# Kernel tuning notes

Measured on AMD Instinct MI355X. Metric: run time of the kernel, lower is better.

The kernel has to match this reference:

```python
import jax, jax.numpy as jnp
import numpy as np

B, N, DIM = 2, 512, 512
HEADS, DIM_HEAD, MAX_LEN = 8, 64, 1024


def _skew(QEr):
    # pad last dim on the left by 1, reshape (n, n+1) -> (n+1, n), drop first row
    padded = jnp.pad(QEr, ((0, 0), (0, 0), (0, 0), (1, 0)))
    b, h, r, c = padded.shape
    return padded.reshape(b, h, c, r)[:, :, 1:, :]


def _fft_multiply_parallel(A, x):
    # A: [b,h,n,n] decay matrix; x: [b,h,n,d]
    b, h, n, d = x.shape
    # y = [last column of A, first row of A] -> [b,h,2n]
    y = jnp.concatenate([A[:, :, :, -1], A[:, :, 0, :]], axis=-1)
    v = jnp.concatenate([x, jnp.zeros_like(x)], axis=-2)  # zero-pad rows n -> 2n
    # Faithful to the original torch code: fftn over ALL axes (incl. batch/head),
    # then ifft over the LAST axis only, then slice back to n rows.
    H = jnp.fft.fftn(y)[:, :, :, None] * jnp.fft.fftn(v)
    return jnp.fft.ifft(H)[:, :, :n, :]


def _forward(x, Wq, Wk, Wv, Er):
    b, n, _ = x.shape

    def split_heads(t):
        return t.reshape(b, n, HEADS, DIM_HEAD).transpose(0, 2, 1, 3)  # [b,h,n,d]

    q = split_heads(x @ Wq)
    k = split_heads(x @ Wk)
    v = split_heads(x @ Wv)
    # global (Frobenius) norm over the full tensor, as torch.norm(t)
    q = q / jnp.linalg.norm(q)
    k = k / jnp.linalg.norm(k)
    q_ = jax.nn.elu(q)
    k_ = jax.nn.elu(k)

    Er_t = Er[MAX_LEN - n:, :].T        # [d, n]
    QEr = q @ Er_t                       # [b,h,n,n]
    c = jnp.exp(_skew(QEr))              # relative-position decay, [b,h,n,n]

    a_1 = jnp.einsum('bhnx,bhny->bhnxy', k_, v).reshape(b, HEADS, n, DIM_HEAD * DIM_HEAD)
    d_2 = _fft_multiply_parallel(c, k_)                                   # [b,h,n,d] complex
    d_1 = _fft_multiply_parallel(c, a_1).reshape(b, HEADS, n, DIM_HEAD, DIM_HEAD)

    top = jnp.einsum('bhnx,bhnyz->bhnz', q_, d_1)    # complex [b,h,n,d]
    bottom = jnp.einsum('bhnx,bhny->bhny', q_, d_2)  # complex [b,h,n,d]
    return top / bottom


def setup_inputs() -> dict:
    key = jax.random.key(0)
    k1, k2, k3, k4, k5 = jax.random.split(key, 5)
    s = jnp.float32(1.0 / np.sqrt(DIM))
    return {
        'x': jax.random.normal(k1, (B, N, DIM), dtype=jnp.float32),
        'Wq': jax.random.normal(k2, (DIM, HEADS * DIM_HEAD), dtype=jnp.float32) * s,
        'Wk': jax.random.normal(k3, (DIM, HEADS * DIM_HEAD), dtype=jnp.float32) * s,
        'Wv': jax.random.normal(k4, (DIM, HEADS * DIM_HEAD), dtype=jnp.float32) * s,
        'Er': jax.random.normal(k5, (MAX_LEN, DIM_HEAD), dtype=jnp.float32),
    }


def reference(x, Wq, Wk, Wv, Er):
    return _forward(x, Wq, Wk, Wv, Er)
```

## Files before the change

kernel.cpp:

```cpp
#include <hip/hip_runtime.h>
#include <math.h>


#define DIMX 512
#define NPOS 512
#define PADIDX(m) ((m) + ((m) >> 4))

typedef unsigned short ushort_t;
typedef unsigned int uint_t;
typedef __bf16 bf16x8 __attribute__((ext_vector_type(8)));
typedef float floatx4 __attribute__((ext_vector_type(4)));

static __device__ inline ushort_t f2bf(float f) {
    uint_t u = __float_as_uint(f);
    u = u + 0x7FFFu + ((u >> 16) & 1u);
    return (ushort_t)(u >> 16);
}
static __device__ inline float bf2f(ushort_t h) {
    return __uint_as_float(((uint_t)h) << 16);
}

__global__ __launch_bounds__(256)
void convx_kernel(const float* __restrict__ x,
                  ushort_t* __restrict__ xh, ushort_t* __restrict__ xl)
{
    const int idx4 = blockIdx.x * 256 + threadIdx.x;
    const float4 v = ((const float4*)x)[idx4];
    ushort_t h[4], l[4];
    const float vf[4] = {v.x, v.y, v.z, v.w};
    #pragma unroll
    for (int e = 0; e < 4; ++e) {
        h[e] = f2bf(vf[e]);
        l[e] = f2bf(vf[e] - bf2f(h[e]));
    }
    ushort_t* ph = xh + (size_t)idx4 * 4;
    ushort_t* pl = xl + (size_t)idx4 * 4;
    #pragma unroll
    for (int e = 0; e < 4; ++e) { ph[e] = h[e]; pl[e] = l[e]; }
}

__global__ __launch_bounds__(256)
void convw_kernel(const float* __restrict__ Wk, const float* __restrict__ Wv,
                  ushort_t* __restrict__ wth, ushort_t* __restrict__ wtl)
{
    const int blk = blockIdx.x;
    const int s  = blk >> 8;
    const int kt = (blk >> 4) & 15;
    const int nt = blk & 15;
    const int t  = threadIdx.x;
    const int c  = t & 31, r4 = t >> 5;
    const float* __restrict__ W = s ? Wv : Wk;
    __shared__ float tile[32][33];

    #pragma unroll
    for (int i = 0; i < 4; ++i) {
        const int row = r4 + i * 8;
        tile[row][c] = W[(size_t)(kt * 32 + row) * 512 + nt * 32 + c];
    }
    __syncthreads();
    #pragma unroll
    for (int i = 0; i < 4; ++i) {
        const int nl = r4 + i * 8;
        const float v = tile[c][nl];
        const ushort_t h = f2bf(v);
        const ushort_t l = f2bf(v - bf2f(h));
        const size_t o = (size_t)(s * 512 + nt * 32 + nl) * 512 + kt * 32 + c;
        wth[o] = h;
        wtl[o] = l;
    }
}

__global__ __launch_bounds__(256)
void gemm_mfma_kernel(const ushort_t* __restrict__ xh, const ushort_t* __restrict__ xl,
                      const ushort_t* __restrict__ wth, const ushort_t* __restrict__ wtl,
                      float* __restrict__ K, float* __restrict__ V,
                      float* __restrict__ partials)
{
    const int blk = blockIdx.x;
    const int ct = blk >> 5;
    const int rt = blk & 31;
    const int t = threadIdx.x;
    const int w = t >> 6, lane = t & 63;
    const int qd = lane >> 4, lm = lane & 15;
    const int mrow  = rt * 32 + (w >> 1) * 16 + lm;
    const int ncol0 = ct * 64 + (w & 1) * 32;
    const size_t aoff  = (size_t)mrow * 512 + qd * 8;
    const size_t boff0 = (size_t)(ncol0 + lm) * 512 + qd * 8;
    const size_t boff1 = (size_t)(ncol0 + 16 + lm) * 512 + qd * 8;

    floatx4 acc0 = {0.f, 0.f, 0.f, 0.f};
    floatx4 acc1 = {0.f, 0.f, 0.f, 0.f};

    #pragma unroll
    for (int ks = 0; ks < 16; ++ks) {
        const int k0 = ks * 32;
        const bf16x8 Ah  = *(const bf16x8*)&xh [aoff  + k0];
        const bf16x8 Al  = *(const bf16x8*)&xl [aoff  + k0];
        const bf16x8 B0h = *(const bf16x8*)&wth[boff0 + k0];
        const bf16x8 B0l = *(const bf16x8*)&wtl[boff0 + k0];
        const bf16x8 B1h = *(const bf16x8*)&wth[boff1 + k0];
        const bf16x8 B1l = *(const bf16x8*)&wtl[boff1 + k0];
        acc0 = __builtin_amdgcn_mfma_f32_16x16x32_bf16(Ah, B0h, acc0, 0, 0, 0);
        acc0 = __builtin_amdgcn_mfma_f32_16x16x32_bf16(Ah, B0l, acc0, 0, 0, 0);
        acc0 = __builtin_amdgcn_mfma_f32_16x16x32_bf16(Al, B0h, acc0, 0, 0, 0);
        acc1 = __builtin_amdgcn_mfma_f32_16x16x32_bf16(Ah, B1h, acc1, 0, 0, 0);
        acc1 = __builtin_amdgcn_mfma_f32_16x16x32_bf16(Ah, B1l, acc1, 0, 0, 0);
        acc1 = __builtin_amdgcn_mfma_f32_16x16x32_bf16(Al, B1h, acc1, 0, 0, 0);
    }

    __shared__ float red[4];
    float ss = 0.f;
    const int orow0 = rt * 32 + (w >> 1) * 16 + qd * 4;
    float* __restrict__ O = (ct < 8) ? K : V;
    const int cb = (ct < 8) ? 0 : 512;
    const int c0 = ncol0 + lm - cb;
    #pragma unroll
    for (int r = 0; r < 4; ++r) {
        const size_t row = orow0 + r;
        const float v0 = acc0[r], v1 = acc1[r];
        O[row * 512 + c0]      = v0;
        O[row * 512 + c0 + 16] = v1;
        if (ct < 8) ss += v0 * v0 + v1 * v1;
    }
    #pragma unroll
    for (int off = 32; off > 0; off >>= 1)
        ss += __shfl_down(ss, off, 64);
    if (lane == 0) red[w] = ss;
    __syncthreads();
    if (t == 0) partials[blk] = red[0] + red[1] + red[2] + red[3];
}

__global__ __launch_bounds__(256)
void gemm_kv_kernel(const float* __restrict__ x,
                    const float* __restrict__ Wk,
                    const float* __restrict__ Wv,
                    float* __restrict__ K,
                    float* __restrict__ V,
                    float* __restrict__ partials)
{
    const int blk  = blockIdx.x;
    const int sel  = (blk >> 2) & 1;
    const int cg   = blk & 3;
    const int rt   = blk >> 3;
    const int row0 = rt * 16;
    const int col0 = cg * 128;
    const int t    = threadIdx.x;
    const int tc   = t & 31;
    const int tr   = t >> 5;
    const float* __restrict__ W   = sel ? Wv : Wk;
    float* __restrict__       Out = sel ? V  : K;

    __shared__ float xs[16][DIMX];
    __shared__ float red[4];

    #pragma unroll
    for (int j = 0; j < 8; ++j) {
        const int f = t + j * 256;
        const int row = f >> 7, c4 = f & 127;
        *(float4*)&xs[row][c4 * 4] = *(const float4*)&x[(size_t)(row0 + row) * DIMX + c4 * 4];
    }
    __syncthreads();

    const float* Wb = W + col0 + tc * 4;
    float4 wA[8], wB[8];
    #pragma unroll
    for (int j = 0; j < 8; ++j) wA[j] = *(const float4*)&Wb[(size_t)(j) * DIMX];
    #pragma unroll
    for (int j = 0; j < 8; ++j) wB[j] = *(const float4*)&Wb[(size_t)(8 + j) * DIMX];

    float acc[2][4] = {{0,0,0,0},{0,0,0,0}};
    const int r0 = tr * 2;

    #define COMPUTE_CHUNK(WREG, CH)                                            \
        {   float4 xv0a = *(const float4*)&xs[r0][(CH) * 8];                   \
            float4 xv0b = *(const float4*)&xs[r0][(CH) * 8 + 4];               \
            float4 xv1a = *(const float4*)&xs[r0 + 1][(CH) * 8];               \
            float4 xv1b = *(const float4*)&xs[r0 + 1][(CH) * 8 + 4];           \
            _Pragma("unroll")                                                  \
            for (int kk = 0; kk < 4; ++kk) {                                   \
                const float x0 = (&xv0a.x)[kk], x1 = (&xv1a.x)[kk];            \
                _Pragma("unroll")                                              \
                for (int cc = 0; cc < 4; ++cc) {                               \
                    acc[0][cc] = fmaf(x0, (&WREG[kk].x)[cc], acc[0][cc]);      \
                    acc[1][cc] = fmaf(x1, (&WREG[kk].x)[cc], acc[1][cc]);      \
                } }                                                            \
            _Pragma("unroll")                                                  \
            for (int kk = 0; kk < 4; ++kk) {                                   \
                const float x0 = (&xv0b.x)[kk], x1 = (&xv1b.x)[kk];            \
                _Pragma("unroll")                                              \
                for (int cc = 0; cc < 4; ++cc) {                               \
                    acc[0][cc] = fmaf(x0, (&WREG[kk + 4].x)[cc], acc[0][cc]);  \
                    acc[1][cc] = fmaf(x1, (&WREG[kk + 4].x)[cc], acc[1][cc]);  \
                } } }

    for (int ch = 0; ch < 64; ch += 2) {
        COMPUTE_CHUNK(wA, ch)
        if (ch < 62) {
            #pragma unroll
            for (int j = 0; j < 8; ++j)
                wA[j] = *(const float4*)&Wb[(size_t)((ch + 2) * 8 + j) * DIMX];
        }
        COMPUTE_CHUNK(wB, ch + 1)
        if (ch < 62) {
            #pragma unroll
            for (int j = 0; j < 8; ++j)
                wB[j] = *(const float4*)&Wb[(size_t)((ch + 3) * 8 + j) * DIMX];
        }
    }
    #undef COMPUTE_CHUNK

    float ss = 0.f;
    #pragma unroll
    for (int i = 0; i < 2; ++i) {
        const int row = row0 + r0 + i;
        const float4 o = make_float4(acc[i][0], acc[i][1], acc[i][2], acc[i][3]);
        *(float4*)&Out[(size_t)row * DIMX + col0 + tc * 4] = o;
        ss += o.x * o.x + o.y * o.y + o.z * o.z + o.w * o.w;
    }
    if (sel == 0) {
        #pragma unroll
        for (int off = 32; off > 0; off >>= 1)
            ss += __shfl_down(ss, off, 64);
        if ((t & 63) == 0) red[t >> 6] = ss;
        __syncthreads();
        if (t == 0) partials[blk] = red[0] + red[1] + red[2] + red[3];
    } else {
        if (t == 0) partials[blk] = 0.f;
    }
}

__device__ __constant__ float C8[8] = {
    1.f, 0.70710678118654752440f, 0.f, -0.70710678118654752440f,
   -1.f, -0.70710678118654752440f, 0.f, 0.70710678118654752440f };
__device__ __constant__ float S8[8] = {
    0.f, -0.70710678118654752440f, -1.f, -0.70710678118654752440f,
    0.f,  0.70710678118654752440f,  1.f,  0.70710678118654752440f };

__global__ __launch_bounds__(256)
void stage1_kernel(const float* __restrict__ K,
                   const float* __restrict__ V,
                   const float* __restrict__ partials,
                   float2* __restrict__ Gk,
                   float2* __restrict__ Gp)
{
    const int m = blockIdx.x;
    const int t = threadIdx.x;
    __shared__ float kk[2][8][64];
    __shared__ float pp[2][8][64];
    __shared__ float skp[16][4];
    __shared__ float sk[2][8];
    __shared__ float sred[4];

    float p = partials[t] + partials[t + 256];
    #pragma unroll
    for (int off = 32; off > 0; off >>= 1)
        p += __shfl_down(p, off, 64);
    if ((t & 63) == 0) sred[t >> 6] = p;
    __syncthreads();
    const float scale = (float)(1.0 / sqrt((double)sred[0] + (double)sred[1] +
                                           (double)sred[2] + (double)sred[3]));

    for (int e = t; e < 1024; e += 256) {
        const int b = e >> 9, rem = e & 511, h = rem >> 6, z = rem & 63;
        const size_t src = (size_t)(b * 512 + m) * DIMX + h * 64 + z;
        const float kv = K[src] * scale;
        kk[b][h][z] = kv > 0.f ? kv : expm1f(kv);
        pp[b][h][z] = V[src];
    }
    __syncthreads();
    if (t < 64) {
        const int bh = t >> 2, q = t & 3;
        float s = 0.f;
        #pragma unroll
        for (int zz = 0; zz < 16; ++zz) s += kk[bh >> 3][bh & 7][q * 16 + zz];
        skp[bh][q] = s;
    }
    __syncthreads();
    if (t < 16) sk[t >> 3][t & 7] = skp[t][0] + skp[t][1] + skp[t][2] + skp[t][3];
    __syncthreads();
    for (int e = t; e < 1024; e += 256) {
        const int b = e >> 9, rem = e & 511, h = rem >> 6, z = rem & 63;
        pp[b][h][z] *= sk[b][h];
    }
    __syncthreads();

    for (int e2 = t; e2 < 512; e2 += 256) {
        const int be = e2 >> 5;
        const int zp = e2 & 31;
        const int beta = be >> 3, eta = be & 7;
        float4 rk, rp;
        #pragma unroll
        for (int zz = 0; zz < 2; ++zz) {
            const int z = zp * 2 + zz;
            float gkr = 0.f, gki = 0.f, gpr = 0.f, gpi = 0.f;
            #pragma unroll
            for (int b = 0; b < 2; ++b) {
                const float sgn = (beta & b) ? -1.f : 1.f;
                #pragma unroll
                for (int h = 0; h < 8; ++h) {
                    const int ph = (eta * h) & 7;
                    const float cr = C8[ph], ci = S8[ph];
                    const float a = kk[b][h][z] * sgn;
                    gkr = fmaf(a, cr, gkr); gki = fmaf(a, ci, gki);
                    const float p2 = pp[b][h][z] * sgn;
                    gpr = fmaf(p2, cr, gpr); gpi = fmaf(p2, ci, gpi);
                }
            }
            if (zz == 0) { rk.x = gkr; rk.y = gki; rp.x = gpr; rp.y = gpi; }
            else         { rk.z = gkr; rk.w = gki; rp.z = gpr; rp.w = gpi; }
        }
        const size_t o = ((size_t)be * NPOS + m) * 64 + zp * 2;
        *(float4*)&Gk[o] = rk;
        *(float4*)&Gp[o] = rp;
    }
}

__global__ __launch_bounds__(256)
void fft_div_kernel(const float2* __restrict__ Gk,
                    const float2* __restrict__ Gp,
                    float* __restrict__ out, int out_cplx)
{
    const int blk = blockIdx.x;
    const int j  = blk & 7;
    const int l  = (blk >> 3) & 3;
    const int be = blk >> 5;
    const int zg = j * 4 + l;
    const int t  = threadIdx.x;

    __shared__ float2 g[4][1088];
    __shared__ float2 w[544];

    for (int jj = t; jj < 512; jj += 256) {
        double s, cc;
        sincos(-6.2831853071795864769 * (double)jj / 1024.0, &s, &cc);
        w[PADIDX(jj)] = make_float2((float)cc, (float)s);
    }
    __syncthreads();

    for (int e = t; e < 1024; e += 256) {
        const int a = e >> 9;
        const int m = e & 511;
        const float4 v4 = *(const float4*)&(a ? Gp : Gk)[((size_t)be * NPOS + m) * 64 + zg * 2];
        const float2 v0 = make_float2(v4.x, v4.y);
        const float2 v1 = make_float2(v4.z, v4.w);
        const float2 tw = w[PADIDX(m)];
        g[a * 2 + 0][PADIDX(m)] = v0;
        g[a * 2 + 1][PADIDX(m)] = v1;
        g[a * 2 + 0][PADIDX(m + 512)] = make_float2(v0.x * tw.x - v0.y * tw.y,
                                                    v0.x * tw.y + v0.y * tw.x);
        g[a * 2 + 1][PADIDX(m + 512)] = make_float2(v1.x * tw.x - v1.y * tw.y,
                                                    v1.x * tw.y + v1.y * tw.x);
    }
    __syncthreads();

    #pragma unroll
    for (int s = 1; s <= 9; ++s) {
        const int S = 512 >> s;
        const int lg = 9 - s;
        #pragma unroll
        for (int q = 0; q < 8; ++q) {
            const int B    = t + 256 * q;
            const int arr  = B >> 9;
            const int beta = B & 511;
            const int jb   = beta & (S - 1);
            const int seg  = beta >> lg;
            const int u    = (seg << (lg + 1)) + jb;
            const int v    = u + S;
            const float2 tw = w[PADIDX(jb << s)];
            const float2 A  = g[arr][PADIDX(u)];
            const float2 Bb = g[arr][PADIDX(v)];
            g[arr][PADIDX(u)] = make_float2(A.x + Bb.x, A.y + Bb.y);
            const float sr = A.x - Bb.x, si = A.y - Bb.y;
            g[arr][PADIDX(v)] = make_float2(sr * tw.x - si * tw.y,
                                            sr * tw.y + si * tw.x);
        }
        __syncthreads();
    }

    for (int e2 = t; e2 < 512; e2 += 256) {
        const int i  = e2;
        const int pi = PADIDX(2 * i);
        const int mu = (int)(__brev((unsigned)i) >> 23);
        float4 res;
        #pragma unroll
        for (int zi = 0; zi < 2; ++zi) {
            const float2 D  = g[zi][pi];
            const float2 Nm = g[2 + zi][pi];
            const float inv = 1.f / (D.x * D.x + D.y * D.y);
            const float rr = (Nm.x * D.x + Nm.y * D.y) * inv;
            const float ri = (Nm.y * D.x - Nm.x * D.y) * inv;
            if (zi == 0) { res.x = rr; res.y = ri; }
            else         { res.z = rr; res.w = ri; }
        }
        const size_t o = ((size_t)be * NPOS + mu) * 64 + zg * 2;
        if (out_cplx) {
            *(float4*)&((float2*)out)[o] = res;
        } else {
            out[o]     = res.x;
            out[o + 1] = res.z;
        }
    }
}

__global__ __launch_bounds__(256)
void mdft_fallback_kernel(const float2* __restrict__ Gk,
                          const float2* __restrict__ Gp,
                          float* __restrict__ out,
                          int out_cplx)
{
    const int blk = blockIdx.x;
    const int be = blk >> 6, z = blk & 63;
    const int t = threadIdx.x;
    __shared__ float2 gk[512];
    __shared__ float2 gp[512];
    __shared__ float2 w[1024];

    for (int m = t; m < 512; m += 256) {
        const size_t idx = ((size_t)be * NPOS + m) * 64 + z;
        gk[m] = Gk[idx];
        gp[m] = Gp[idx];
    }
    for (int jj = t; jj < 1024; jj += 256) {
        double s, c;
        sincos(-6.2831853071795864769 * (double)jj / 1024.0, &s, &c);
        w[jj] = make_float2((float)c, (float)s);
    }
    __syncthreads();

    #pragma unroll
    for (int half = 0; half < 2; ++half) {
        const int mu = t + half * 256;
        double dr = 0.0, di = 0.0, nr = 0.0, ni = 0.0;
        int idx = 0;
        for (int m = 0; m < 512; ++m) {
            const float2 tw = w[idx];
            idx = (idx + mu) & 1023;
            const float2 a = gk[m];
            dr += (double)(a.x * tw.x - a.y * tw.y);
            di += (double)(a.x * tw.y + a.y * tw.x);
            const float2 p = gp[m];
            nr += (double)(p.x * tw.x - p.y * tw.y);
            ni += (double)(p.x * tw.y + p.y * tw.x);
        }
        const double dmag = dr * dr + di * di;
        const double orr = (nr * dr + ni * di) / dmag;
        const double oii = (ni * dr - nr * di) / dmag;
        const size_t o = ((size_t)be * NPOS + mu) * 64 + z;
        if (out_cplx) {
            out[2 * o]     = (float)orr;
            out[2 * o + 1] = (float)oii;
        } else {
            out[o] = (float)orr;
        }
    }
}

extern "C" void kernel_launch(void* const* d_in, const int* in_sizes, int n_in,
                              void* d_out, int out_size, void* d_ws, size_t ws_size,
                              hipStream_t stream)
{
    const float* x  = (const float*)d_in[0];
    const float* Wk = (const float*)d_in[2];
    const float* Wv = (const float*)d_in[3];
    float* out = (float*)d_out;

    char* ws = (char*)d_ws;
    float*  K    = (float*)(ws);
    float*  V    = (float*)(ws + (size_t)2097152);
    float2* Gk   = (float2*)(ws + (size_t)4194304);
    float*  part = (float*)(ws + (size_t)8388608);
    const int out_cplx = (out_size >= 2 * 2 * 8 * 512 * 64) ? 1 : 0;

    const bool ws_big = (ws_size >= (size_t)20971520);
    float2* Gp = ws_big ? (float2*)(ws + (size_t)8390656)
                        : (float2*)d_out;

    if (ws_big) {
        ushort_t* xh  = (ushort_t*)(ws + (size_t)16777216);
        ushort_t* xl  = (ushort_t*)(ws + (size_t)17825792);
        ushort_t* wth = (ushort_t*)(ws + (size_t)18874368);
        ushort_t* wtl = (ushort_t*)(ws + (size_t)19922944);
        hipLaunchKernelGGL(convx_kernel, dim3(512), dim3(256), 0, stream,
                           x, xh, xl);
        hipLaunchKernelGGL(convw_kernel, dim3(512), dim3(256), 0, stream,
                           Wk, Wv, wth, wtl);
        hipLaunchKernelGGL(gemm_mfma_kernel, dim3(512), dim3(256), 0, stream,
                           xh, xl, wth, wtl, K, V, part);
        hipLaunchKernelGGL(stage1_kernel, dim3(512), dim3(256), 0, stream,
                           K, V, part, Gk, Gp);
        hipLaunchKernelGGL(fft_div_kernel, dim3(512), dim3(256), 0, stream,
                           Gk, Gp, out, out_cplx);
    } else {
        hipLaunchKernelGGL(gemm_kv_kernel, dim3(512), dim3(256), 0, stream,
                           x, Wk, Wv, K, V, part);
        hipLaunchKernelGGL(stage1_kernel, dim3(512), dim3(256), 0, stream,
                           K, V, part, Gk, Gp);
        hipLaunchKernelGGL(mdft_fallback_kernel, dim3(1024), dim3(256), 0, stream,
                           Gk, Gp, out, out_cplx);
    }
}
```

Before: 113.0 us.

## Fuse five-stage pipeline into one cooperative kernel with grid syncs

Merges the conversion, MFMA GEMM, stage1 and FFT-divide kernels into a single cooperative kernel that separates phases with grid-wide syncs and shares one statically sized shared-memory buffer. The aim is to remove four kernel launch gaps and their inter-kernel drain and refill. The trade-off is that every phase now runs under the largest shared-memory footprint and register budget, and grid.sync adds its own barrier cost. If the cooperative launch fails, the code falls back to the original separate launches.

```diff
diff --git a/kernel.cpp b/kernel.cpp
--- a/kernel.cpp
+++ b/kernel.cpp
@@ -1,10 +1,14 @@
 #include <hip/hip_runtime.h>
+#include <hip/hip_cooperative_groups.h>
 #include <math.h>
+
+namespace cg = cooperative_groups;
 
 
 #define DIMX 512
 #define NPOS 512
 #define PADIDX(m) ((m) + ((m) >> 4))
+#define SM_BYTES 39168
 
 typedef unsigned short ushort_t;
 typedef unsigned int uint_t;
@@ -20,14 +24,22 @@
     return __uint_as_float(((uint_t)h) << 16);
 }
 
-__global__ __launch_bounds__(256)
-void convx_kernel(const float* __restrict__ x,
-                  ushort_t* __restrict__ xh, ushort_t* __restrict__ xl)
-{
-    const int idx4 = blockIdx.x * 256 + threadIdx.x;
+__device__ __constant__ float C8[8] = {
+    1.f, 0.70710678118654752440f, 0.f, -0.70710678118654752440f,
+   -1.f, -0.70710678118654752440f, 0.f, 0.70710678118654752440f };
+__device__ __constant__ float S8[8] = {
+    0.f, -0.70710678118654752440f, -1.f, -0.70710678118654752440f,
+    0.f,  0.70710678118654752440f,  1.f,  0.70710678118654752440f };
+
+static __device__ inline void phase_convx(const float* __restrict__ x,
+                                          ushort_t* __restrict__ xh,
+                                          ushort_t* __restrict__ xl,
+                                          int blk, int t)
+{
+    const int idx4 = blk * 256 + t;
     const float4 v = ((const float4*)x)[idx4];
+    const float vf[4] = {v.x, v.y, v.z, v.w};
     ushort_t h[4], l[4];
-    const float vf[4] = {v.x, v.y, v.z, v.w};
     #pragma unroll
     for (int e = 0; e < 4; ++e) {
         h[e] = f2bf(vf[e]);
@@ -39,19 +51,18 @@
     for (int e = 0; e < 4; ++e) { ph[e] = h[e]; pl[e] = l[e]; }
 }
 
-__global__ __launch_bounds__(256)
-void convw_kernel(const float* __restrict__ Wk, const float* __restrict__ Wv,
-                  ushort_t* __restrict__ wth, ushort_t* __restrict__ wtl)
-{
-    const int blk = blockIdx.x;
+static __device__ inline void phase_convw(const float* __restrict__ Wk,
+                                          const float* __restrict__ Wv,
+                                          ushort_t* __restrict__ wth,
+                                          ushort_t* __restrict__ wtl,
+                                          int blk, int t, char* smraw)
+{
+    float (*tile)[33] = (float(*)[33])smraw;
     const int s  = blk >> 8;
     const int kt = (blk >> 4) & 15;
     const int nt = blk & 15;
-    const int t  = threadIdx.x;
     const int c  = t & 31, r4 = t >> 5;
     const float* __restrict__ W = s ? Wv : Wk;
-    __shared__ float tile[32][33];
-
     #pragma unroll
     for (int i = 0; i < 4; ++i) {
         const int row = r4 + i * 8;
@@ -70,16 +81,18 @@
     }
 }
 
-__global__ __launch_bounds__(256)
-void gemm_mfma_kernel(const ushort_t* __restrict__ xh, const ushort_t* __restrict__ xl,
-                      const ushort_t* __restrict__ wth, const ushort_t* __restrict__ wtl,
-                      float* __restrict__ K, float* __restrict__ V,
-                      float* __restrict__ partials)
-{
-    const int blk = blockIdx.x;
+static __device__ inline void phase_gemm(const ushort_t* __restrict__ xh,
+                                         const ushort_t* __restrict__ xl,
+                                         const ushort_t* __restrict__ wth,
+                                         const ushort_t* __restrict__ wtl,
+                                         float* __restrict__ K,
+                                         float* __restrict__ V,
+                                         float* __restrict__ partials,
+                                         int blk, int t, char* smraw)
+{
+    float* red = (float*)smraw;
     const int ct = blk >> 5;
     const int rt = blk & 31;
-    const int t = threadIdx.x;
     const int w = t >> 6, lane = t & 63;
     const int qd = lane >> 4, lm = lane & 15;
     const int mrow  = rt * 32 + (w >> 1) * 16 + lm;
@@ -108,7 +121,6 @@
         acc1 = __builtin_amdgcn_mfma_f32_16x16x32_bf16(Al, B1h, acc1, 0, 0, 0);
     }
 
-    __shared__ float red[4];
     float ss = 0.f;
     const int orow0 = rt * 32 + (w >> 1) * 16 + qd * 4;
     float* __restrict__ O = (ct < 8) ? K : V;
@@ -130,126 +142,18 @@
     if (t == 0) partials[blk] = red[0] + red[1] + red[2] + red[3];
 }
 
-__global__ __launch_bounds__(256)
-void gemm_kv_kernel(const float* __restrict__ x,
-                    const float* __restrict__ Wk,
-                    const float* __restrict__ Wv,
-                    float* __restrict__ K,
-                    float* __restrict__ V,
-                    float* __restrict__ partials)
-{
-    const int blk  = blockIdx.x;
-    const int sel  = (blk >> 2) & 1;
-    const int cg   = blk & 3;
-    const int rt   = blk >> 3;
-    const int row0 = rt * 16;
-    const int col0 = cg * 128;
-    const int t    = threadIdx.x;
-    const int tc   = t & 31;
-    const int tr   = t >> 5;
-    const float* __restrict__ W   = sel ? Wv : Wk;
-    float* __restrict__       Out = sel ? V  : K;
-
-    __shared__ float xs[16][DIMX];
-    __shared__ float red[4];
-
-    #pragma unroll
-    for (int j = 0; j < 8; ++j) {
-        const int f = t + j * 256;
-        const int row = f >> 7, c4 = f & 127;
-        *(float4*)&xs[row][c4 * 4] = *(const float4*)&x[(size_t)(row0 + row) * DIMX + c4 * 4];
-    }
-    __syncthreads();
-
-    const float* Wb = W + col0 + tc * 4;
-    float4 wA[8], wB[8];
-    #pragma unroll
-    for (int j = 0; j < 8; ++j) wA[j] = *(const float4*)&Wb[(size_t)(j) * DIMX];
-    #pragma unroll
-    for (int j = 0; j < 8; ++j) wB[j] = *(const float4*)&Wb[(size_t)(8 + j) * DIMX];
-
-    float acc[2][4] = {{0,0,0,0},{0,0,0,0}};
-    const int r0 = tr * 2;
-
-    #define COMPUTE_CHUNK(WREG, CH)                                            \
-        {   float4 xv0a = *(const float4*)&xs[r0][(CH) * 8];                   \
-            float4 xv0b = *(const float4*)&xs[r0][(CH) * 8 + 4];               \
-            float4 xv1a = *(const float4*)&xs[r0 + 1][(CH) * 8];               \
-            float4 xv1b = *(const float4*)&xs[r0 + 1][(CH) * 8 + 4];           \
-            _Pragma("unroll")                                                  \
-            for (int kk = 0; kk < 4; ++kk) {                                   \
-                const float x0 = (&xv0a.x)[kk], x1 = (&xv1a.x)[kk];            \
-                _Pragma("unroll")                                              \
-                for (int cc = 0; cc < 4; ++cc) {                               \
-                    acc[0][cc] = fmaf(x0, (&WREG[kk].x)[cc], acc[0][cc]);      \
-                    acc[1][cc] = fmaf(x1, (&WREG[kk].x)[cc], acc[1][cc]);      \
-                } }                                                            \
-            _Pragma("unroll")                                                  \
-            for (int kk = 0; kk < 4; ++kk) {                                   \
-                const float x0 = (&xv0b.x)[kk], x1 = (&xv1b.x)[kk];            \
-                _Pragma("unroll")                                              \
-                for (int cc = 0; cc < 4; ++cc) {                               \
-                    acc[0][cc] = fmaf(x0, (&WREG[kk + 4].x)[cc], acc[0][cc]);  \
-                    acc[1][cc] = fmaf(x1, (&WREG[kk + 4].x)[cc], acc[1][cc]);  \
-                } } }
-
-    for (int ch = 0; ch < 64; ch += 2) {
-        COMPUTE_CHUNK(wA, ch)
-        if (ch < 62) {
-            #pragma unroll
-            for (int j = 0; j < 8; ++j)
-                wA[j] = *(const float4*)&Wb[(size_t)((ch + 2) * 8 + j) * DIMX];
-        }
-        COMPUTE_CHUNK(wB, ch + 1)
-        if (ch < 62) {
-            #pragma unroll
-            for (int j = 0; j < 8; ++j)
-                wB[j] = *(const float4*)&Wb[(size_t)((ch + 3) * 8 + j) * DIMX];
-        }
-    }
-    #undef COMPUTE_CHUNK
-
-    float ss = 0.f;
-    #pragma unroll
-    for (int i = 0; i < 2; ++i) {
-        const int row = row0 + r0 + i;
-        const float4 o = make_float4(acc[i][0], acc[i][1], acc[i][2], acc[i][3]);
-        *(float4*)&Out[(size_t)row * DIMX + col0 + tc * 4] = o;
-        ss += o.x * o.x + o.y * o.y + o.z * o.z + o.w * o.w;
-    }
-    if (sel == 0) {
-        #pragma unroll
-        for (int off = 32; off > 0; off >>= 1)
-            ss += __shfl_down(ss, off, 64);
-        if ((t & 63) == 0) red[t >> 6] = ss;
-        __syncthreads();
-        if (t == 0) partials[blk] = red[0] + red[1] + red[2] + red[3];
-    } else {
-        if (t == 0) partials[blk] = 0.f;
-    }
-}
-
-__device__ __constant__ float C8[8] = {
-    1.f, 0.70710678118654752440f, 0.f, -0.70710678118654752440f,
-   -1.f, -0.70710678118654752440f, 0.f, 0.70710678118654752440f };
-__device__ __constant__ float S8[8] = {
-    0.f, -0.70710678118654752440f, -1.f, -0.70710678118654752440f,
-    0.f,  0.70710678118654752440f,  1.f,  0.70710678118654752440f };
-
-__global__ __launch_bounds__(256)
-void stage1_kernel(const float* __restrict__ K,
-                   const float* __restrict__ V,
-                   const float* __restrict__ partials,
-                   float2* __restrict__ Gk,
-                   float2* __restrict__ Gp)
-{
-    const int m = blockIdx.x;
-    const int t = threadIdx.x;
-    __shared__ float kk[2][8][64];
-    __shared__ float pp[2][8][64];
-    __shared__ float skp[16][4];
-    __shared__ float sk[2][8];
-    __shared__ float sred[4];
+static __device__ inline void phase_stage1(const float* __restrict__ K,
+                                           const float* __restrict__ V,
+                                           const float* __restrict__ partials,
+                                           float2* __restrict__ Gk,
+                                           float2* __restrict__ Gp,
+                                           int m, int t, char* smraw)
+{
+    float (*kk)[8][64] = (float(*)[8][64])(smraw);
+    float (*pp)[8][64] = (float(*)[8][64])(smraw + 4096);
+    float (*skp)[4]    = (float(*)[4])(smraw + 8192);
+    float (*sk)[8]     = (float(*)[8])(smraw + 8448);
+    float* sred        = (float*)(smraw + 8512);
 
     float p = partials[t] + partials[t + 256];
     #pragma unroll
@@ -315,20 +219,18 @@
     }
 }
 
-__global__ __launch_bounds__(256)
-void fft_div_kernel(const float2* __restrict__ Gk,
-                    const float2* __restrict__ Gp,
-                    float* __restrict__ out, int out_cplx)
-{
-    const int blk = blockIdx.x;
+static __device__ inline void phase_fft(const float2* __restrict__ Gk,
+                                        const float2* __restrict__ Gp,
+                                        float* __restrict__ out, int out_cplx,
+                                        int blk, int t, char* smraw)
+{
+    float2 (*g)[1088] = (float2(*)[1088])smraw;
+    float2* w = (float2*)(smraw + 34816);
+
     const int j  = blk & 7;
     const int l  = (blk >> 3) & 3;
     const int be = blk >> 5;
     const int zg = j * 4 + l;
-    const int t  = threadIdx.x;
-
-    __shared__ float2 g[4][1088];
-    __shared__ float2 w[544];
 
     for (int jj = t; jj < 512; jj += 256) {
         double s, cc;
@@ -402,6 +304,169 @@
     }
 }
 
+__global__ __launch_bounds__(256, 2)
+void fused_kernel(const float* __restrict__ x,
+                  const float* __restrict__ Wk, const float* __restrict__ Wv,
+                  ushort_t* __restrict__ xh, ushort_t* __restrict__ xl,
+                  ushort_t* __restrict__ wth, ushort_t* __restrict__ wtl,
+                  float* __restrict__ K, float* __restrict__ V,
+                  float* __restrict__ partials,
+                  float2* __restrict__ Gk, float2* __restrict__ Gp,
+                  float* __restrict__ out, int out_cplx)
+{
+    cg::grid_group grid = cg::this_grid();
+    __shared__ __align__(16) char smraw[SM_BYTES];
+    const int blk = blockIdx.x;
+    const int t = threadIdx.x;
+    phase_convx(x, xh, xl, blk, t);
+    phase_convw(Wk, Wv, wth, wtl, blk, t, smraw);
+    grid.sync();
+    phase_gemm(xh, xl, wth, wtl, K, V, partials, blk, t, smraw);
+    grid.sync();
+    phase_stage1(K, V, partials, Gk, Gp, blk, t, smraw);
+    grid.sync();
+    phase_fft(Gk, Gp, out, out_cplx, blk, t, smraw);
+}
+
+__global__ __launch_bounds__(256)
+void convx_kernel(const float* __restrict__ x,
+                  ushort_t* __restrict__ xh, ushort_t* __restrict__ xl)
+{ phase_convx(x, xh, xl, blockIdx.x, threadIdx.x); }
+
+__global__ __launch_bounds__(256)
+void convw_kernel(const float* __restrict__ Wk, const float* __restrict__ Wv,
+                  ushort_t* __restrict__ wth, ushort_t* __restrict__ wtl)
+{
+    __shared__ __align__(16) char sm[4224];
+    phase_convw(Wk, Wv, wth, wtl, blockIdx.x, threadIdx.x, sm);
+}
+
+__global__ __launch_bounds__(256)
+void gemm_mfma_kernel(const ushort_t* __restrict__ xh, const ushort_t* __restrict__ xl,
+                      const ushort_t* __restrict__ wth, const ushort_t* __restrict__ wtl,
+                      float* __restrict__ K, float* __restrict__ V,
+                      float* __restrict__ partials)
+{
+    __shared__ __align__(16) char sm[16];
+    phase_gemm(xh, xl, wth, wtl, K, V, partials, blockIdx.x, threadIdx.x, sm);
+}
+
+__global__ __launch_bounds__(256)
+void stage1_kernel(const float* __restrict__ K, const float* __restrict__ V,
+                   const float* __restrict__ partials,
+                   float2* __restrict__ Gk, float2* __restrict__ Gp)
+{
+    __shared__ __align__(16) char sm[8528];
+    phase_stage1(K, V, partials, Gk, Gp, blockIdx.x, threadIdx.x, sm);
+}
+
+__global__ __launch_bounds__(256)
+void fft_div_kernel(const float2* __restrict__ Gk, const float2* __restrict__ Gp,
+                    float* __restrict__ out, int out_cplx)
+{
+    __shared__ __align__(16) char sm[SM_BYTES];
+    phase_fft(Gk, Gp, out, out_cplx, blockIdx.x, threadIdx.x, sm);
+}
+
+__global__ __launch_bounds__(256)
+void gemm_kv_kernel(const float* __restrict__ x,
+                    const float* __restrict__ Wk,
+                    const float* __restrict__ Wv,
+                    float* __restrict__ K,
+                    float* __restrict__ V,
+                    float* __restrict__ partials)
+{
+    const int blk  = blockIdx.x;
+    const int sel  = (blk >> 2) & 1;
+    const int cg2  = blk & 3;
+    const int rt   = blk >> 3;
+    const int row0 = rt * 16;
+    const int col0 = cg2 * 128;
+    const int t    = threadIdx.x;
+    const int tc   = t & 31;
+    const int tr   = t >> 5;
+    const float* __restrict__ W   = sel ? Wv : Wk;
+    float* __restrict__       Out = sel ? V  : K;
+
+    __shared__ float xs[16][DIMX];
+    __shared__ float red[4];
+
+    #pragma unroll
+    for (int j = 0; j < 8; ++j) {
+        const int f = t + j * 256;
+        const int row = f >> 7, c4 = f & 127;
+        *(float4*)&xs[row][c4 * 4] = *(const float4*)&x[(size_t)(row0 + row) * DIMX + c4 * 4];
+    }
+    __syncthreads();
+
+    const float* Wb = W + col0 + tc * 4;
+    float4 wA[8], wB[8];
+    #pragma unroll
+    for (int j = 0; j < 8; ++j) wA[j] = *(const float4*)&Wb[(size_t)(j) * DIMX];
+    #pragma unroll
+    for (int j = 0; j < 8; ++j) wB[j] = *(const float4*)&Wb[(size_t)(8 + j) * DIMX];
+
+    float acc[2][4] = {{0,0,0,0},{0,0,0,0}};
+    const int r0 = tr * 2;
+
+    #define COMPUTE_CHUNK(WREG, CH)                                            \
+        {   float4 xv0a = *(const float4*)&xs[r0][(CH) * 8];                   \
+            float4 xv0b = *(const float4*)&xs[r0][(CH) * 8 + 4];               \
+            float4 xv1a = *(const float4*)&xs[r0 + 1][(CH) * 8];               \
+            float4 xv1b = *(const float4*)&xs[r0 + 1][(CH) * 8 + 4];           \
+            _Pragma("unroll")                                                  \
+            for (int kk = 0; kk < 4; ++kk) {                                   \
+                const float x0 = (&xv0a.x)[kk], x1 = (&xv1a.x)[kk];            \
+                _Pragma("unroll")                                              \
+                for (int cc = 0; cc < 4; ++cc) {                               \
+                    acc[0][cc] = fmaf(x0, (&WREG[kk].x)[cc], acc[0][cc]);      \
+                    acc[1][cc] = fmaf(x1, (&WREG[kk].x)[cc], acc[1][cc]);      \
+                } }                                                            \
+            _Pragma("unroll")                                                  \
+            for (int kk = 0; kk < 4; ++kk) {                                   \
+                const float x0 = (&xv0b.x)[kk], x1 = (&xv1b.x)[kk];            \
+                _Pragma("unroll")                                              \
+                for (int cc = 0; cc < 4; ++cc) {                               \
+                    acc[0][cc] = fmaf(x0, (&WREG[kk + 4].x)[cc], acc[0][cc]);  \
+                    acc[1][cc] = fmaf(x1, (&WREG[kk + 4].x)[cc], acc[1][cc]);  \
+                } } }
+
+    for (int ch = 0; ch < 64; ch += 2) {
+        COMPUTE_CHUNK(wA, ch)
+        if (ch < 62) {
+            #pragma unroll
+            for (int j = 0; j < 8; ++j)
+                wA[j] = *(const float4*)&Wb[(size_t)((ch + 2) * 8 + j) * DIMX];
+        }
+        COMPUTE_CHUNK(wB, ch + 1)
+        if (ch < 62) {
+            #pragma unroll
+            for (int j = 0; j < 8; ++j)
+                wB[j] = *(const float4*)&Wb[(size_t)((ch + 3) * 8 + j) * DIMX];
+        }
+    }
+    #undef COMPUTE_CHUNK
+
+    float ss = 0.f;
+    #pragma unroll
+    for (int i = 0; i < 2; ++i) {
+        const int row = row0 + r0 + i;
+        const float4 o = make_float4(acc[i][0], acc[i][1], acc[i][2], acc[i][3]);
+        *(float4*)&Out[(size_t)row * DIMX + col0 + tc * 4] = o;
+        ss += o.x * o.x + o.y * o.y + o.z * o.z + o.w * o.w;
+    }
+    if (sel == 0) {
+        #pragma unroll
+        for (int off = 32; off > 0; off >>= 1)
+            ss += __shfl_down(ss, off, 64);
+        if ((t & 63) == 0) red[t >> 6] = ss;
+        __syncthreads();
+        if (t == 0) partials[blk] = red[0] + red[1] + red[2] + red[3];
+    } else {
+        if (t == 0) partials[blk] = 0.f;
+    }
+}
+
 __global__ __launch_bounds__(256)
 void mdft_fallback_kernel(const float2* __restrict__ Gk,
                           const float2* __restrict__ Gp,
@@ -480,16 +545,30 @@
         ushort_t* xl  = (ushort_t*)(ws + (size_t)17825792);
         ushort_t* wth = (ushort_t*)(ws + (size_t)18874368);
         ushort_t* wtl = (ushort_t*)(ws + (size_t)19922944);
-        hipLaunchKernelGGL(convx_kernel, dim3(512), dim3(256), 0, stream,
-                           x, xh, xl);
-        hipLaunchKernelGGL(convw_kernel, dim3(512), dim3(256), 0, stream,
-                           Wk, Wv, wth, wtl);
-        hipLaunchKernelGGL(gemm_mfma_kernel, dim3(512), dim3(256), 0, stream,
-                           xh, xl, wth, wtl, K, V, part);
-        hipLaunchKernelGGL(stage1_kernel, dim3(512), dim3(256), 0, stream,
-                           K, V, part, Gk, Gp);
-        hipLaunchKernelGGL(fft_div_kernel, dim3(512), dim3(256), 0, stream,
-                           Gk, Gp, out, out_cplx);
+
+        const float* xa = x; const float* wka = Wk; const float* wva = Wv;
+        ushort_t* xha = xh; ushort_t* xla = xl;
+        ushort_t* wtha = wth; ushort_t* wtla = wtl;
+        float* Ka = K; float* Va = V; float* pa = part;
+        float2* Gka = Gk; float2* Gpa = Gp; float* oa = out;
+        int oc = out_cplx;
+        void* args[] = { &xa, &wka, &wva, &xha, &xla, &wtha, &wtla,
+                         &Ka, &Va, &pa, &Gka, &Gpa, &oa, &oc };
+        hipError_t err = hipLaunchCooperativeKernel(
+            (const void*)fused_kernel, dim3(512), dim3(256), args, 0, stream);
+        if (err != hipSuccess) {
+            (void)hipGetLastError();
+            hipLaunchKernelGGL(convx_kernel, dim3(512), dim3(256), 0, stream,
+                               x, xh, xl);
+            hipLaunchKernelGGL(convw_kernel, dim3(512), dim3(256), 0, stream,
+                               Wk, Wv, wth, wtl);
+            hipLaunchKernelGGL(gemm_mfma_kernel, dim3(512), dim3(256), 0, stream,
+                               xh, xl, wth, wtl, K, V, part);
+            hipLaunchKernelGGL(stage1_kernel, dim3(512), dim3(256), 0, stream,
+                               K, V, part, Gk, Gp);
+            hipLaunchKernelGGL(fft_div_kernel, dim3(512), dim3(256), 0, stream,
+                               Gk, Gp, out, out_cplx);
+        }
     } else {
         hipLaunchKernelGGL(gemm_kv_kernel, dim3(512), dim3(256), 0, stream,
                            x, Wk, Wv, K, V, part);
```

Measured after the change: 283.4 us. 2.51x slower.
